# Performance work log

Hardware: AMD Instinct MI355X
Metric: run time of the kernel (lower is better)

Reference implementation:

```python
import jax, jax.numpy as jnp
import numpy as np

IN_CH = 256
OUT_CH = 128
N = 6144
ADJ_P = 0.01  # edge density -> avg degree ~61


def setup_inputs() -> dict:
    key = jax.random.key(0)
    ks = jax.random.split(key, 8)
    x = jax.random.normal(ks[0], (1, IN_CH, N), dtype=jnp.float32)
    adj = (jax.random.uniform(ks[1], (N, N)) < ADJ_P).astype(jnp.float32)
    W_fts = jax.random.normal(ks[2], (OUT_CH, IN_CH), dtype=jnp.float32) * 0.05
    w1 = jax.random.normal(ks[3], (OUT_CH,), dtype=jnp.float32) * 0.05
    b1 = jnp.zeros((1,), dtype=jnp.float32)
    w2 = jax.random.normal(ks[4], (OUT_CH,), dtype=jnp.float32) * 0.05
    b2 = jnp.zeros((1,), dtype=jnp.float32)
    vars_bias = jax.random.normal(ks[5], (1, N, OUT_CH), dtype=jnp.float32) * 0.02
    return {"x": x, "adj": adj, "W_fts": W_fts, "w1": w1, "b1": b1,
            "w2": w2, "b2": b2, "vars_bias": vars_bias}


def reference(x, adj, W_fts, w1, b1, w2, b2, vars_bias):
    # fts = Conv1d(in, out, k=1, bias=False)(x): [1, OUT_CH, N]
    fts = jnp.einsum('oi,bin->bon', W_fts, x)
    f = fts[0]  # [OUT_CH, N]
    # f1/f2 = Conv1d(out, 1, 1)(fts) -> per-node scalars [N]
    f1 = jnp.einsum('o,on->n', w1, f) + b1  # [N]
    f2 = jnp.einsum('o,on->n', w2, f) + b2  # [N]
    # scores[i,j] = leaky_relu(adj[i,j]*f1[i] + adj[i,j]*f2[j], 0.2)
    scores = jax.nn.leaky_relu(adj * f1[:, None] + adj * f2[None, :], 0.2)
    # sparse_softmax2d: per-row softmax masked to nonzero entries
    mask = (scores != 0).astype(scores.dtype)
    m = jnp.max(scores, axis=1, keepdims=True)  # stabilizer; cancels in ratio
    exps = jnp.exp(scores - m) * mask
    coefs = exps / jnp.sum(exps, axis=1, keepdims=True)  # [N, N]
    # vals = coefs @ fts.T : [N, OUT_CH]
    vals = coefs @ f.T
    # add bias, permute to [1, OUT_CH, N]
    ret = jnp.transpose(vals[None, :, :] + vars_bias, (0, 2, 1))
    return ret
```

## Files before the change

kernel.cpp:

```cpp
#include <hip/hip_runtime.h>

#define NN  6144
#define ICH 256
#define OCH 128
#define QW  160

typedef float vf4 __attribute__((ext_vector_type(4)));

__global__ __launch_bounds__(256) void k_fts(const float* __restrict__ x,
        const float* __restrict__ W, const float* __restrict__ w1,
        const float* __restrict__ w2, float* __restrict__ ft,
        float* __restrict__ f1, float* __restrict__ f2) {
    __shared__ float xs[32][32];
    __shared__ float Ws[32][OCH + 4];
    const int n0  = blockIdx.x * 32;
    const int tid = threadIdx.x;
    const int oq = (tid & 31) * 4;
    const int nq = (tid >> 5) * 4;
    float acc[4][4] = {};
    for (int k0 = 0; k0 < ICH; k0 += 32) {
        __syncthreads();
        {
            const int nn = tid & 31;
            const int kb = tid >> 5;
#pragma unroll
            for (int r = 0; r < 4; ++r)
                xs[kb + r * 8][nn] = x[(size_t)(k0 + kb + r * 8) * NN + n0 + nn];
        }
        {
            const int kk = tid & 31;
            const int ob = tid >> 5;
#pragma unroll
            for (int r = 0; r < 16; ++r) {
                const int o = ob + r * 8;
                Ws[kk][o] = W[o * ICH + k0 + kk];
            }
        }
        __syncthreads();
#pragma unroll
        for (int kk = 0; kk < 32; ++kk) {
            const float4 xv = *(const float4*)&xs[kk][nq];
            const float4 wv = *(const float4*)&Ws[kk][oq];
            const float xa[4] = {xv.x, xv.y, xv.z, xv.w};
            const float wa[4] = {wv.x, wv.y, wv.z, wv.w};
#pragma unroll
            for (int a = 0; a < 4; ++a)
#pragma unroll
                for (int b = 0; b < 4; ++b)
                    acc[a][b] = fmaf(xa[a], wa[b], acc[a][b]);
        }
    }
#pragma unroll
    for (int a = 0; a < 4; ++a) {
        float4 v = make_float4(acc[a][0], acc[a][1], acc[a][2], acc[a][3]);
        *(float4*)&ft[(size_t)(n0 + nq + a) * OCH + oq] = v;
    }
    const float4 w1v = *(const float4*)(w1 + oq);
    const float4 w2v = *(const float4*)(w2 + oq);
    float p1[4], p2[4];
#pragma unroll
    for (int a = 0; a < 4; ++a) {
        p1[a] = acc[a][0] * w1v.x + acc[a][1] * w1v.y + acc[a][2] * w1v.z + acc[a][3] * w1v.w;
        p2[a] = acc[a][0] * w2v.x + acc[a][1] * w2v.y + acc[a][2] * w2v.z + acc[a][3] * w2v.w;
    }
#pragma unroll
    for (int m = 16; m > 0; m >>= 1) {
#pragma unroll
        for (int a = 0; a < 4; ++a) {
            p1[a] += __shfl_xor(p1[a], m);
            p2[a] += __shfl_xor(p2[a], m);
        }
    }
    if ((tid & 31) == 0) {
#pragma unroll
        for (int a = 0; a < 4; ++a) {
            f1[n0 + nq + a] = p1[a];
            f2[n0 + nq + a] = p2[a];
        }
    }
}

__global__ __launch_bounds__(256) void k_attn(const float* __restrict__ adj,
        const float* __restrict__ ft, const float* __restrict__ f1,
        const float* __restrict__ f2, const float* __restrict__ b1,
        const float* __restrict__ b2, const float* __restrict__ vb,
        float* __restrict__ out) {
    __shared__ float q_e[4][QW];
    __shared__ int   q_j[4][QW];
    __shared__ int   qc[4];
    const int tid  = threadIdx.x;
    const int lane = tid & 63;
    const int wave = tid >> 6;
    const int i = blockIdx.x * 4 + wave;
    if (lane == 0) qc[wave] = 0;
    const float s1 = f1[i] + b1[0] + b2[0];
    const float* arow = adj + (size_t)i * NN;
    float den = 0.f;
    vf4 ab[2][6];
#pragma unroll
    for (int w = 0; w < 6; ++w)
        ab[0][w] = __builtin_nontemporal_load((const vf4*)(arow + lane * 4 + w * 256));
#pragma unroll
    for (int b = 0; b < 4; ++b) {
        if (b < 3) {
#pragma unroll
            for (int w = 0; w < 6; ++w)
                ab[(b + 1) & 1][w] = __builtin_nontemporal_load(
                    (const vf4*)(arow + (b + 1) * 1536 + lane * 4 + w * 256));
        }
#pragma unroll
        for (int w = 0; w < 6; ++w) {
            const vf4 a4 = ab[b & 1][w];
            const int j0 = b * 1536 + w * 256 + lane * 4;
            const int k = (a4.x != 0.f) + (a4.y != 0.f) + (a4.z != 0.f) + (a4.w != 0.f);
            if (k) {
                const float4 g = *(const float4*)(f2 + j0);
                int slot = atomicAdd(&qc[wave], k);
                if (slot + k <= QW) {
                    if (a4.x != 0.f) { float s = s1 + g.x; s = s > 0.f ? s : 0.2f * s;
                                       float e = __expf(s); den += e;
                                       q_j[wave][slot] = j0;     q_e[wave][slot] = e; ++slot; }
                    if (a4.y != 0.f) { float s = s1 + g.y; s = s > 0.f ? s : 0.2f * s;
                                       float e = __expf(s); den += e;
                                       q_j[wave][slot] = j0 + 1; q_e[wave][slot] = e; ++slot; }
                    if (a4.z != 0.f) { float s = s1 + g.z; s = s > 0.f ? s : 0.2f * s;
                                       float e = __expf(s); den += e;
                                       q_j[wave][slot] = j0 + 2; q_e[wave][slot] = e; ++slot; }
                    if (a4.w != 0.f) { float s = s1 + g.w; s = s > 0.f ? s : 0.2f * s;
                                       float e = __expf(s); den += e;
                                       q_j[wave][slot] = j0 + 3; q_e[wave][slot] = e; }
                }
            }
        }
    }
#pragma unroll
    for (int off = 32; off > 0; off >>= 1) den += __shfl_xor(den, off);
    const float inv = 1.f / den;
    const int nE = qc[wave] < QW ? qc[wave] : QW;
    const int half = lane >> 5;
    const int c0 = (lane & 31) * 4;
    float4 nm = make_float4(0.f, 0.f, 0.f, 0.f);
#pragma unroll 2
    for (int idx = half; idx < nE; idx += 2) {
        const int   j = q_j[wave][idx];
        const float e = q_e[wave][idx];
        const float4 g = *(const float4*)(ft + (size_t)j * OCH + c0);
        nm.x = fmaf(e, g.x, nm.x);
        nm.y = fmaf(e, g.y, nm.y);
        nm.z = fmaf(e, g.z, nm.z);
        nm.w = fmaf(e, g.w, nm.w);
    }
    nm.x += __shfl_xor(nm.x, 32);
    nm.y += __shfl_xor(nm.y, 32);
    nm.z += __shfl_xor(nm.z, 32);
    nm.w += __shfl_xor(nm.w, 32);
    if (half == 0) {
        const float4 bv = *(const float4*)(vb + (size_t)i * OCH + c0);
        out[(size_t)(c0    ) * NN + i] = fmaf(nm.x, inv, bv.x);
        out[(size_t)(c0 + 1) * NN + i] = fmaf(nm.y, inv, bv.y);
        out[(size_t)(c0 + 2) * NN + i] = fmaf(nm.z, inv, bv.z);
        out[(size_t)(c0 + 3) * NN + i] = fmaf(nm.w, inv, bv.w);
    }
}

extern "C" void kernel_launch(void* const* d_in, const int* in_sizes, int n_in,
                              void* d_out, int out_size, void* d_ws, size_t ws_size,
                              hipStream_t stream) {
    const float* x   = (const float*)d_in[0];
    const float* adj = (const float*)d_in[1];
    const float* W   = (const float*)d_in[2];
    const float* w1  = (const float*)d_in[3];
    const float* b1  = (const float*)d_in[4];
    const float* w2  = (const float*)d_in[5];
    const float* b2  = (const float*)d_in[6];
    const float* vb  = (const float*)d_in[7];
    float* out = (float*)d_out;

    char* ws = (char*)d_ws;
    float* ft = (float*)ws;
    float* f1 = (float*)(ws + 3145728);
    float* f2 = (float*)(ws + 3145728 + 24576);

    k_fts<<<dim3(NN / 32), 256, 0, stream>>>(x, W, w1, w2, ft, f1, f2);
    k_attn<<<dim3(NN / 4), 256, 0, stream>>>(adj, ft, f1, f2, b1, b2, vb, out);
}
```

Before: 261.4 us.

## Split attention into row-parallel scan and gather kernels with global edge buffers

The fused per-row attention kernel becomes two kernels. A scan kernel assigns one block per row, with each wave scanning a quarter of the adjacency row, and writes compacted (index, exp) pairs, counts and partial denominators to workspace. A gather kernel then has each wave accumulate its quarter's weighted features, and the partials are reduced through shared memory. This gives more parallelism per row and removes the serial 4-chunk loop per wave, at the cost of an extra launch and a global round-trip for the edge lists. Each quarter's queue is capped at 64 entries, which could drop edges on rows that are unusually dense.

```diff
diff --git a/kernel.cpp b/kernel.cpp
--- a/kernel.cpp
+++ b/kernel.cpp
@@ -3,9 +3,7 @@
 #define NN  6144
 #define ICH 256
 #define OCH 128
-#define QW  160
-
-typedef float vf4 __attribute__((ext_vector_type(4)));
+#define QC  64
 
 __global__ __launch_bounds__(256) void k_fts(const float* __restrict__ x,
         const float* __restrict__ W, const float* __restrict__ w1,
@@ -80,70 +78,77 @@
     }
 }
 
-__global__ __launch_bounds__(256) void k_attn(const float* __restrict__ adj,
-        const float* __restrict__ ft, const float* __restrict__ f1,
-        const float* __restrict__ f2, const float* __restrict__ b1,
-        const float* __restrict__ b2, const float* __restrict__ vb,
-        float* __restrict__ out) {
-    __shared__ float q_e[4][QW];
-    __shared__ int   q_j[4][QW];
-    __shared__ int   qc[4];
+__global__ __launch_bounds__(256) void k_scan(const float* __restrict__ adj,
+        const float* __restrict__ f1, const float* __restrict__ f2,
+        const float* __restrict__ b1, const float* __restrict__ b2,
+        float2* __restrict__ eb, int* __restrict__ cnt,
+        float* __restrict__ dens) {
+    __shared__ int qc[4];
     const int tid  = threadIdx.x;
     const int lane = tid & 63;
     const int wave = tid >> 6;
-    const int i = blockIdx.x * 4 + wave;
+    const int i = blockIdx.x;
     if (lane == 0) qc[wave] = 0;
     const float s1 = f1[i] + b1[0] + b2[0];
     const float* arow = adj + (size_t)i * NN;
-    float den = 0.f;
-    vf4 ab[2][6];
+    const int qbase = (i * 4 + wave) * QC;
+    float4 a[6];
 #pragma unroll
     for (int w = 0; w < 6; ++w)
-        ab[0][w] = __builtin_nontemporal_load((const vf4*)(arow + lane * 4 + w * 256));
+        a[w] = *(const float4*)(arow + wave * 1536 + w * 256 + lane * 4);
+    float den = 0.f;
 #pragma unroll
-    for (int b = 0; b < 4; ++b) {
-        if (b < 3) {
-#pragma unroll
-            for (int w = 0; w < 6; ++w)
-                ab[(b + 1) & 1][w] = __builtin_nontemporal_load(
-                    (const vf4*)(arow + (b + 1) * 1536 + lane * 4 + w * 256));
-        }
-#pragma unroll
-        for (int w = 0; w < 6; ++w) {
-            const vf4 a4 = ab[b & 1][w];
-            const int j0 = b * 1536 + w * 256 + lane * 4;
-            const int k = (a4.x != 0.f) + (a4.y != 0.f) + (a4.z != 0.f) + (a4.w != 0.f);
-            if (k) {
-                const float4 g = *(const float4*)(f2 + j0);
-                int slot = atomicAdd(&qc[wave], k);
-                if (slot + k <= QW) {
-                    if (a4.x != 0.f) { float s = s1 + g.x; s = s > 0.f ? s : 0.2f * s;
-                                       float e = __expf(s); den += e;
-                                       q_j[wave][slot] = j0;     q_e[wave][slot] = e; ++slot; }
-                    if (a4.y != 0.f) { float s = s1 + g.y; s = s > 0.f ? s : 0.2f * s;
-                                       float e = __expf(s); den += e;
-                                       q_j[wave][slot] = j0 + 1; q_e[wave][slot] = e; ++slot; }
-                    if (a4.z != 0.f) { float s = s1 + g.z; s = s > 0.f ? s : 0.2f * s;
-                                       float e = __expf(s); den += e;
-                                       q_j[wave][slot] = j0 + 2; q_e[wave][slot] = e; ++slot; }
-                    if (a4.w != 0.f) { float s = s1 + g.w; s = s > 0.f ? s : 0.2f * s;
-                                       float e = __expf(s); den += e;
-                                       q_j[wave][slot] = j0 + 3; q_e[wave][slot] = e; }
-                }
+    for (int w = 0; w < 6; ++w) {
+        const float4 a4 = a[w];
+        const int j0 = wave * 1536 + w * 256 + lane * 4;
+        const int k = (a4.x != 0.f) + (a4.y != 0.f) + (a4.z != 0.f) + (a4.w != 0.f);
+        if (k) {
+            const float4 g = *(const float4*)(f2 + j0);
+            int slot = atomicAdd(&qc[wave], k);
+            if (slot + k <= QC) {
+                if (a4.x != 0.f) { float s = s1 + g.x; s = s > 0.f ? s : 0.2f * s;
+                                   float e = __expf(s); den += e;
+                                   eb[qbase + slot] = make_float2(__int_as_float(j0), e); ++slot; }
+                if (a4.y != 0.f) { float s = s1 + g.y; s = s > 0.f ? s : 0.2f * s;
+                                   float e = __expf(s); den += e;
+                                   eb[qbase + slot] = make_float2(__int_as_float(j0 + 1), e); ++slot; }
+                if (a4.z != 0.f) { float s = s1 + g.z; s = s > 0.f ? s : 0.2f * s;
+                                   float e = __expf(s); den += e;
+                                   eb[qbase + slot] = make_float2(__int_as_float(j0 + 2), e); ++slot; }
+                if (a4.w != 0.f) { float s = s1 + g.w; s = s > 0.f ? s : 0.2f * s;
+                                   float e = __expf(s); den += e;
+                                   eb[qbase + slot] = make_float2(__int_as_float(j0 + 3), e); }
             }
         }
     }
 #pragma unroll
     for (int off = 32; off > 0; off >>= 1) den += __shfl_xor(den, off);
-    const float inv = 1.f / den;
-    const int nE = qc[wave] < QW ? qc[wave] : QW;
+    const int total = qc[wave];
+    if (lane == 0) {
+        cnt[i * 4 + wave]  = total < QC ? total : QC;
+        dens[i * 4 + wave] = den;
+    }
+}
+
+__global__ __launch_bounds__(256) void k_gather(const float2* __restrict__ eb,
+        const int* __restrict__ cnt, const float* __restrict__ dens,
+        const float* __restrict__ ft, const float* __restrict__ vb,
+        float* __restrict__ out) {
+    __shared__ float part[4][OCH];
+    const int tid  = threadIdx.x;
+    const int lane = tid & 63;
+    const int wave = tid >> 6;
+    const int i = blockIdx.x;
+    const int c = cnt[i * 4 + wave];
+    const int qbase = (i * 4 + wave) * QC;
     const int half = lane >> 5;
     const int c0 = (lane & 31) * 4;
     float4 nm = make_float4(0.f, 0.f, 0.f, 0.f);
 #pragma unroll 2
-    for (int idx = half; idx < nE; idx += 2) {
-        const int   j = q_j[wave][idx];
-        const float e = q_e[wave][idx];
+    for (int idx = half; idx < c; idx += 2) {
+        const float2 pe = eb[qbase + idx];
+        const int   j = __float_as_int(pe.x);
+        const float e = pe.y;
         const float4 g = *(const float4*)(ft + (size_t)j * OCH + c0);
         nm.x = fmaf(e, g.x, nm.x);
         nm.y = fmaf(e, g.y, nm.y);
@@ -154,12 +159,15 @@
     nm.y += __shfl_xor(nm.y, 32);
     nm.z += __shfl_xor(nm.z, 32);
     nm.w += __shfl_xor(nm.w, 32);
-    if (half == 0) {
-        const float4 bv = *(const float4*)(vb + (size_t)i * OCH + c0);
-        out[(size_t)(c0    ) * NN + i] = fmaf(nm.x, inv, bv.x);
-        out[(size_t)(c0 + 1) * NN + i] = fmaf(nm.y, inv, bv.y);
-        out[(size_t)(c0 + 2) * NN + i] = fmaf(nm.z, inv, bv.z);
-        out[(size_t)(c0 + 3) * NN + i] = fmaf(nm.w, inv, bv.w);
+    if (half == 0)
+        *(float4*)&part[wave][c0] = nm;
+    __syncthreads();
+    if (tid < OCH) {
+        const float den = dens[i * 4] + dens[i * 4 + 1]
+                        + dens[i * 4 + 2] + dens[i * 4 + 3];
+        const float inv = 1.f / den;
+        const float v = part[0][tid] + part[1][tid] + part[2][tid] + part[3][tid];
+        out[(size_t)tid * NN + i] = fmaf(v, inv, vb[(size_t)i * OCH + tid]);
     }
 }
 
@@ -177,10 +185,14 @@
     float* out = (float*)d_out;
 
     char* ws = (char*)d_ws;
-    float* ft = (float*)ws;
-    float* f1 = (float*)(ws + 3145728);
-    float* f2 = (float*)(ws + 3145728 + 24576);
+    float*  ft   = (float*)ws;
+    float*  f1   = (float*)(ws + 3145728);
+    float*  f2   = (float*)(ws + 3145728 + 24576);
+    float2* eb   = (float2*)(ws + 3194880);
+    int*    cnt  = (int*)  (ws + 3194880 + 12582912);
+    float*  dens = (float*)(ws + 3194880 + 12582912 + 98304);
 
     k_fts<<<dim3(NN / 32), 256, 0, stream>>>(x, W, w1, w2, ft, f1, f2);
-    k_attn<<<dim3(NN / 4), 256, 0, stream>>>(adj, ft, f1, f2, b1, b2, vb, out);
+    k_scan<<<dim3(NN), 256, 0, stream>>>(adj, f1, f2, b1, b2, eb, cnt, dens);
+    k_gather<<<dim3(NN), 256, 0, stream>>>(eb, cnt, dens, ft, vb, out);
 }
```

New measurement: 287.2 us. 1.1x slower.

## Split adjacency scan into bitmask kernel and ballot-compacted edge kernel

Applied to the files above, without the earlier changes.

Adds a kernel that streams the dense adjacency matrix once and packs it into a per-row bitmask. The attention kernel then reads only the bitmask and compacts edges with wave ballot and prefix popcount, replacing the shared-memory atomic counter. The edge index and weight are packed into one float2 shared array, and the gather loop is unrolled further. The split is meant to decouple the bandwidth-bound adjacency read from the latency-bound gather, at the cost of an extra launch and a small mask round-trip through memory.

```diff
diff --git a/kernel.cpp b/kernel.cpp
--- a/kernel.cpp
+++ b/kernel.cpp
@@ -80,75 +80,85 @@
     }
 }
 
-__global__ __launch_bounds__(256) void k_attn(const float* __restrict__ adj,
+__global__ __launch_bounds__(256) void k_mask(const float* __restrict__ adj,
+        unsigned* __restrict__ mask) {
+    const int lane = threadIdx.x & 63;
+    const int wave = threadIdx.x >> 6;
+    const int u = blockIdx.x * 4 + wave;
+    const int i = u / 3;
+    const int g = u - i * 3;
+    const float* p = adj + (size_t)i * NN + g * 2048 + lane * 4;
+    vf4 a[8];
+#pragma unroll
+    for (int k = 0; k < 8; ++k)
+        a[k] = *(const vf4*)(p + k * 256);
+    unsigned w = 0;
+#pragma unroll
+    for (int k = 0; k < 8; ++k) {
+        w |= (a[k].x != 0.f ? 1u : 0u) << (4 * k);
+        w |= (a[k].y != 0.f ? 2u : 0u) << (4 * k);
+        w |= (a[k].z != 0.f ? 4u : 0u) << (4 * k);
+        w |= (a[k].w != 0.f ? 8u : 0u) << (4 * k);
+    }
+    mask[(size_t)(i * 3 + g) * 64 + lane] = w;
+}
+
+__global__ __launch_bounds__(256) void k_edge(const unsigned* __restrict__ mask,
         const float* __restrict__ ft, const float* __restrict__ f1,
         const float* __restrict__ f2, const float* __restrict__ b1,
         const float* __restrict__ b2, const float* __restrict__ vb,
         float* __restrict__ out) {
-    __shared__ float q_e[4][QW];
-    __shared__ int   q_j[4][QW];
-    __shared__ int   qc[4];
+    __shared__ float2 q[4][QW];
     const int tid  = threadIdx.x;
     const int lane = tid & 63;
     const int wave = tid >> 6;
     const int i = blockIdx.x * 4 + wave;
-    if (lane == 0) qc[wave] = 0;
     const float s1 = f1[i] + b1[0] + b2[0];
-    const float* arow = adj + (size_t)i * NN;
+    unsigned mw[3];
+#pragma unroll
+    for (int g = 0; g < 3; ++g)
+        mw[g] = mask[(size_t)(i * 3 + g) * 64 + lane];
+    const unsigned long long lt = (1ull << lane) - 1;
     float den = 0.f;
-    vf4 ab[2][6];
+    int cnt = 0;
 #pragma unroll
-    for (int w = 0; w < 6; ++w)
-        ab[0][w] = __builtin_nontemporal_load((const vf4*)(arow + lane * 4 + w * 256));
-#pragma unroll
-    for (int b = 0; b < 4; ++b) {
-        if (b < 3) {
-#pragma unroll
-            for (int w = 0; w < 6; ++w)
-                ab[(b + 1) & 1][w] = __builtin_nontemporal_load(
-                    (const vf4*)(arow + (b + 1) * 1536 + lane * 4 + w * 256));
-        }
-#pragma unroll
-        for (int w = 0; w < 6; ++w) {
-            const vf4 a4 = ab[b & 1][w];
-            const int j0 = b * 1536 + w * 256 + lane * 4;
-            const int k = (a4.x != 0.f) + (a4.y != 0.f) + (a4.z != 0.f) + (a4.w != 0.f);
-            if (k) {
-                const float4 g = *(const float4*)(f2 + j0);
-                int slot = atomicAdd(&qc[wave], k);
-                if (slot + k <= QW) {
-                    if (a4.x != 0.f) { float s = s1 + g.x; s = s > 0.f ? s : 0.2f * s;
-                                       float e = __expf(s); den += e;
-                                       q_j[wave][slot] = j0;     q_e[wave][slot] = e; ++slot; }
-                    if (a4.y != 0.f) { float s = s1 + g.y; s = s > 0.f ? s : 0.2f * s;
-                                       float e = __expf(s); den += e;
-                                       q_j[wave][slot] = j0 + 1; q_e[wave][slot] = e; ++slot; }
-                    if (a4.z != 0.f) { float s = s1 + g.z; s = s > 0.f ? s : 0.2f * s;
-                                       float e = __expf(s); den += e;
-                                       q_j[wave][slot] = j0 + 2; q_e[wave][slot] = e; ++slot; }
-                    if (a4.w != 0.f) { float s = s1 + g.w; s = s > 0.f ? s : 0.2f * s;
-                                       float e = __expf(s); den += e;
-                                       q_j[wave][slot] = j0 + 3; q_e[wave][slot] = e; }
-                }
+    for (int g = 0; g < 3; ++g) {
+        unsigned w = mw[g];
+        for (;;) {
+            const unsigned long long act = __ballot(w != 0);
+            if (!act) break;
+            if (w) {
+                const int b = __builtin_ctz(w);
+                w &= w - 1;
+                const int j = g * 2048 + (b >> 2) * 256 + lane * 4 + (b & 3);
+                float s = s1 + f2[j];
+                s = s > 0.f ? s : 0.2f * s;
+                const float e = __expf(s);
+                den += e;
+                const int slot = cnt + (int)__popcll(act & lt);
+                if (slot < QW)
+                    q[wave][slot] = make_float2(__int_as_float(j), e);
             }
+            cnt += (int)__popcll(act);
         }
     }
 #pragma unroll
     for (int off = 32; off > 0; off >>= 1) den += __shfl_xor(den, off);
     const float inv = 1.f / den;
-    const int nE = qc[wave] < QW ? qc[wave] : QW;
+    const int nE = cnt < QW ? cnt : QW;
     const int half = lane >> 5;
     const int c0 = (lane & 31) * 4;
     float4 nm = make_float4(0.f, 0.f, 0.f, 0.f);
-#pragma unroll 2
+#pragma unroll 4
     for (int idx = half; idx < nE; idx += 2) {
-        const int   j = q_j[wave][idx];
-        const float e = q_e[wave][idx];
-        const float4 g = *(const float4*)(ft + (size_t)j * OCH + c0);
-        nm.x = fmaf(e, g.x, nm.x);
-        nm.y = fmaf(e, g.y, nm.y);
-        nm.z = fmaf(e, g.z, nm.z);
-        nm.w = fmaf(e, g.w, nm.w);
+        const float2 pe = q[wave][idx];
+        const int   j = __float_as_int(pe.x);
+        const float e = pe.y;
+        const float4 g4 = *(const float4*)(ft + (size_t)j * OCH + c0);
+        nm.x = fmaf(e, g4.x, nm.x);
+        nm.y = fmaf(e, g4.y, nm.y);
+        nm.z = fmaf(e, g4.z, nm.z);
+        nm.w = fmaf(e, g4.w, nm.w);
     }
     nm.x += __shfl_xor(nm.x, 32);
     nm.y += __shfl_xor(nm.y, 32);
@@ -177,10 +187,12 @@
     float* out = (float*)d_out;
 
     char* ws = (char*)d_ws;
-    float* ft = (float*)ws;
-    float* f1 = (float*)(ws + 3145728);
-    float* f2 = (float*)(ws + 3145728 + 24576);
+    float*    ft   = (float*)ws;
+    float*    f1   = (float*)(ws + 3145728);
+    float*    f2   = (float*)(ws + 3145728 + 24576);
+    unsigned* mask = (unsigned*)(ws + 3194880);
 
     k_fts<<<dim3(NN / 32), 256, 0, stream>>>(x, W, w1, w2, ft, f1, f2);
-    k_attn<<<dim3(NN / 4), 256, 0, stream>>>(adj, ft, f1, f2, b1, b2, vb, out);
+    k_mask<<<dim3(NN * 3 / 4), 256, 0, stream>>>(adj, mask);
+    k_edge<<<dim3(NN / 4), 256, 0, stream>>>(mask, ft, f1, f2, b1, b2, vb, out);
 }
```

Measured after the change: 274.8 us. 5.1% more time.
